# Kernel tuning notes

Hardware: AMD Instinct MI355X
Metric: run time of the kernel (lower is better)

The kernel has to match this reference:

```python
import jax, jax.numpy as jnp
import numpy as np

NEG_BIG = -(2.0 ** 32) + 1.0  # padding value used in Normal_attention


def setup_inputs() -> dict:
    key = jax.random.key(0)
    ks = jax.random.split(key, 9)
    U, V, kIL, kUI, B, L = 100000, 100001, 64, 64, 16384, 50
    IL = jax.random.normal(ks[0], (4, V, kIL), jnp.float32) * 0.01
    IL = IL.at[:, -1, :].set(0.0)  # padding_idx=-1 row zeroed
    LI = jax.random.normal(ks[1], (4, V, kIL), jnp.float32)
    LI = LI.at[:, -1, :].set(0.0)
    UI = jax.random.normal(ks[2], (4, U, kUI), jnp.float32)
    IU = jax.random.normal(ks[3], (V, kUI), jnp.float32) * 0.01
    IU = IU.at[-1, :].set(0.0)
    alpha = jnp.full((4,), 0.5, jnp.float32)
    uid = jax.random.randint(ks[4], (B,), 0, U)
    baskets = jax.random.randint(ks[5], (4, B, L), 0, V - 1)
    iid = jax.random.randint(ks[6], (4, B), 0, V - 1)
    neg_iid = jax.random.randint(ks[7], (4, B), 0, V - 1)
    return dict(IL=IL, LI=LI, UI=UI, IU=IU, alpha=alpha,
                uid=uid, baskets=baskets, iid=iid, neg_iid=neg_iid)


def _attend_score(x, tgt):
    # x: [B,4,k] aggregated period sequence; tgt: [P,B,k] target item embeddings
    k = x.shape[-1]
    w = jnp.einsum('bsk,pbk->pbs', x, tgt) / jnp.sqrt(jnp.asarray(k, x.dtype))
    w = jnp.where(w == 0.0, jnp.asarray(NEG_BIG, x.dtype), w)  # mask exact zeros (padding)
    w = jax.nn.softmax(w, axis=-1)                              # softmax over seq dim (4)
    # multiply input by attention weight, then bmm with target and sum over seq
    return jnp.einsum('bsk,pbs,pbk->pb', x, w, tgt)


def reference(IL, LI, UI, IU, alpha, uid, baskets, iid, neg_iid):
    n_items = LI.shape[1] - 1
    # aggregate: mean-pool each period's basket embedding -> [B,4,k]
    emb = jax.vmap(lambda W, idx: W[idx])(LI, baskets)          # [4,B,L,k]
    pad_mask = (baskets != n_items)[..., None].astype(emb.dtype)
    x = jnp.transpose(jnp.mean(emb * pad_mask, axis=2), (1, 0, 2))  # [B,4,k]

    tgt_pos = jax.vmap(lambda W, idx: W[idx])(IL, iid)          # [4,B,k]
    tgt_neg = jax.vmap(lambda W, idx: W[idx])(IL, neg_iid)      # [4,B,k]
    attn_pos = _attend_score(x, tgt_pos)                        # [4,B]
    attn_neg = _attend_score(x, tgt_neg)

    u = jax.vmap(lambda W: W[uid])(UI)                          # [4,B,kUI]
    mf_pos = jnp.sum(u * IU[iid], axis=-1)                      # [4,B]
    mf_neg = jnp.sum(u * IU[neg_iid], axis=-1)

    s = jax.nn.sigmoid(alpha)[:, None]                          # [4,1]
    pos = s * attn_pos + (1.0 - s) * mf_pos
    neg = s * attn_neg + (1.0 - s) * mf_neg
    return (pos[0], neg[0], pos[1], neg[1], pos[2], neg[2], pos[3], neg[3])
```

## Files before the change

### kernel.cpp

```cpp
#include <hip/hip_runtime.h>
#include <hip/hip_bf16.h>
#include <math.h>


#define NEG_BIG_F (-4294967295.0f)

typedef float v2f __attribute__((ext_vector_type(2)));

template<int CTRL, int RM>
__device__ __forceinline__ float dpp_add(float v) {
    int moved = __builtin_amdgcn_update_dpp(0, __float_as_int(v), CTRL, RM, 0xf, false);
    return v + __int_as_float(moved);
}

__device__ __forceinline__ float rsum64(float v) {
    v = dpp_add<0x121, 0xf>(v);
    v = dpp_add<0x122, 0xf>(v);
    v = dpp_add<0x124, 0xf>(v);
    v = dpp_add<0x128, 0xf>(v);
    v = dpp_add<0x142, 0xa>(v);
    v = dpp_add<0x143, 0xc>(v);
    return __int_as_float(__builtin_amdgcn_readlane(__float_as_int(v), 63));
}

__device__ __forceinline__ float plswap_add32(float a, float b) {
    auto r = __builtin_amdgcn_permlane32_swap(__float_as_uint(a), __float_as_uint(b),
                                              false, false);
    return __uint_as_float(r[0]) + __uint_as_float(r[1]);
}
__device__ __forceinline__ float plswap_add16(float a, float b) {
    auto r = __builtin_amdgcn_permlane16_swap(__float_as_uint(a), __float_as_uint(b),
                                              false, false);
    return __uint_as_float(r[0]) + __uint_as_float(r[1]);
}

__global__ __launch_bounds__(256) void convert_li_fp8(
    const float* __restrict__ src, unsigned int* __restrict__ dst, long n8)
{
    long i = (long)blockIdx.x * blockDim.x + threadIdx.x;
    const long stride = (long)gridDim.x * blockDim.x;
    for (; i < n8; i += stride) {
        float4 a = ((const float4*)src)[2 * i];
        float4 b = ((const float4*)src)[2 * i + 1];
        int w0 = __builtin_amdgcn_cvt_pk_fp8_f32(a.x, a.y, 0, false);
        w0     = __builtin_amdgcn_cvt_pk_fp8_f32(a.z, a.w, w0, true);
        int w1 = __builtin_amdgcn_cvt_pk_fp8_f32(b.x, b.y, 0, false);
        w1     = __builtin_amdgcn_cvt_pk_fp8_f32(b.z, b.w, w1, true);
        int2 o; o.x = w0; o.y = w1;
        ((int2*)dst)[i] = o;
    }
}

template<bool USE_FP8>
__global__ __launch_bounds__(256) void neuraltmt_kernel(
    const float* __restrict__ IL, const float* __restrict__ LI,
    const float* __restrict__ UI, const float* __restrict__ IU,
    const float* __restrict__ alpha,
    const int* __restrict__ uid, const int* __restrict__ baskets,
    const int* __restrict__ iid, const int* __restrict__ neg_iid,
    const unsigned char* __restrict__ T,
    float* __restrict__ out,
    int Bn, int V, int Ln, int U)
{
    const int b    = blockIdx.x;
    const int lane = threadIdx.x & 63;
    const int w    = threadIdx.x >> 6;
    const int n_items = V - 1;

    __shared__ float xs[4][64];

    const int* bk = baskets + ((size_t)w * Bn + b) * (size_t)Ln;

    if (USE_FP8 && Ln <= 64) {
        const unsigned char* Ts = T + (size_t)w * V * 64;
        int my_idx = (lane < Ln) ? bk[lane] : n_items;
        const int rs = lane >> 3;
        const int kq = lane & 7;

        int2 q[8];
        #pragma unroll
        for (int j = 0; j < 8; ++j) {
            if (8 * j < Ln) {
                int idx = __shfl(my_idx, 8 * j + rs, 64);
                q[j] = *(const int2*)(Ts + (((size_t)(unsigned)idx) << 6) + (kq << 3));
            }
        }
        float acc[8] = {0.f,0.f,0.f,0.f,0.f,0.f,0.f,0.f};
        #pragma unroll
        for (int j = 0; j < 8; ++j) {
            if (8 * j < Ln) {
                v2f d0 = __builtin_amdgcn_cvt_pk_f32_fp8(q[j].x, false);
                v2f d1 = __builtin_amdgcn_cvt_pk_f32_fp8(q[j].x, true);
                v2f d2 = __builtin_amdgcn_cvt_pk_f32_fp8(q[j].y, false);
                v2f d3 = __builtin_amdgcn_cvt_pk_f32_fp8(q[j].y, true);
                acc[0] += d0.x; acc[1] += d0.y; acc[2] += d1.x; acc[3] += d1.y;
                acc[4] += d2.x; acc[5] += d2.y; acc[6] += d3.x; acc[7] += d3.y;
            }
        }
        float s0 = plswap_add32(acc[0], acc[1]);
        float s1 = plswap_add32(acc[2], acc[3]);
        float s2 = plswap_add32(acc[4], acc[5]);
        float s3 = plswap_add32(acc[6], acc[7]);
        float t0 = plswap_add16(s0, s1);
        float t1 = plswap_add16(s2, s3);
        t0 = dpp_add<0x128, 0xf>(t0);
        t1 = dpp_add<0x128, 0xf>(t1);
        if (((lane >> 3) & 1) == 0) {
            const float invL = 1.0f / (float)Ln;
            const int g  = (lane >> 4) & 3;
            const int Ag = ((g & 1) << 1) | (g >> 1);
            const int kb = ((lane & 7) << 3) + Ag;
            xs[w][kb]     = t0 * invL;
            xs[w][kb + 4] = t1 * invL;
        }
    } else {
        const float* LIs = LI + (size_t)w * V * 64;
        const int rq = lane >> 4, kq = lane & 15;
        int my_idx = (lane < Ln && lane < 64) ? bk[lane] : n_items;
        float4 acc = make_float4(0.f, 0.f, 0.f, 0.f);
        const int lcap    = (Ln < 64) ? Ln : 64;
        const int ngroups = (lcap + 3) >> 2;
        int g = 0;
        for (; g + 4 <= ngroups; g += 4) {
            float4 v[4];
            #pragma unroll
            for (int j = 0; j < 4; ++j) {
                int idx = __shfl(my_idx, 4 * (g + j) + rq, 64);
                v[j] = *(const float4*)(LIs + (((size_t)(unsigned)idx) << 6) + (kq << 2));
            }
            #pragma unroll
            for (int j = 0; j < 4; ++j) {
                acc.x += v[j].x; acc.y += v[j].y; acc.z += v[j].z; acc.w += v[j].w;
            }
        }
        for (; g < ngroups; ++g) {
            int idx = __shfl(my_idx, 4 * g + rq, 64);
            float4 vv = *(const float4*)(LIs + (((size_t)(unsigned)idx) << 6) + (kq << 2));
            acc.x += vv.x; acc.y += vv.y; acc.z += vv.z; acc.w += vv.w;
        }
        for (int l = 64; l < Ln; ++l) {
            int idx = bk[l];
            float4 vv = *(const float4*)(LIs + (((size_t)(unsigned)idx) << 6) + (kq << 2));
            float m = (rq == 0) ? 1.0f : 0.0f;
            acc.x += m * vv.x; acc.y += m * vv.y; acc.z += m * vv.z; acc.w += m * vv.w;
        }
        #pragma unroll
        for (int off = 16; off <= 32; off <<= 1) {
            acc.x += __shfl_xor(acc.x, off, 64);
            acc.y += __shfl_xor(acc.y, off, 64);
            acc.z += __shfl_xor(acc.z, off, 64);
            acc.w += __shfl_xor(acc.w, off, 64);
        }
        if (lane < 16) {
            const float invL = 1.0f / (float)Ln;
            float4 xv = make_float4(acc.x * invL, acc.y * invL, acc.z * invL, acc.w * invL);
            *(float4*)&xs[w][lane << 2] = xv;
        }
    }
    __syncthreads();

    const int p = w;
    const float a  = alpha[p];
    const float sg = 1.0f / (1.0f + expf(-a));

    const int ip  = iid[(size_t)p * Bn + b];
    const int in_ = neg_iid[(size_t)p * Bn + b];
    const int u   = uid[b];

    const float* ILp = IL + (size_t)p * V * 64;
    const float tpos = ILp[(size_t)ip  * 64 + lane];
    const float tneg = ILp[(size_t)in_ * 64 + lane];
    const float uv   = UI[((size_t)p * U + u) * 64 + lane];
    const float iup  = IU[(size_t)ip  * 64 + lane];
    const float iun  = IU[(size_t)in_ * 64 + lane];

    float dpos[4], dneg[4];
    #pragma unroll
    for (int s = 0; s < 4; ++s) {
        float xv = xs[s][lane];
        dpos[s] = rsum64(xv * tpos);
        dneg[s] = rsum64(xv * tneg);
    }

    auto attend = [&](const float d[4]) -> float {
        float wv[4], m = -INFINITY;
        #pragma unroll
        for (int s = 0; s < 4; ++s) {
            wv[s] = (d[s] == 0.0f) ? NEG_BIG_F : d[s] * 0.125f;
            m = fmaxf(m, wv[s]);
        }
        float den = 0.0f, num = 0.0f;
        #pragma unroll
        for (int s = 0; s < 4; ++s) {
            float e = expf(wv[s] - m);
            den += e;
            num += e * d[s];
        }
        return num / den;
    };
    const float attn_pos = attend(dpos);
    const float attn_neg = attend(dneg);

    float mp = rsum64(uv * iup);
    float mn = rsum64(uv * iun);

    if (lane == 0) {
        float pos = sg * attn_pos + (1.0f - sg) * mp;
        float neg = sg * attn_neg + (1.0f - sg) * mn;
        out[(size_t)(2 * p)     * Bn + b] = pos;
        out[(size_t)(2 * p + 1) * Bn + b] = neg;
    }
}

extern "C" void kernel_launch(void* const* d_in, const int* in_sizes, int n_in,
                              void* d_out, int out_size, void* d_ws, size_t ws_size,
                              hipStream_t stream) {
    const float* IL      = (const float*)d_in[0];
    const float* LI      = (const float*)d_in[1];
    const float* UI      = (const float*)d_in[2];
    const float* IU      = (const float*)d_in[3];
    const float* alpha   = (const float*)d_in[4];
    const int*   uid     = (const int*)d_in[5];
    const int*   baskets = (const int*)d_in[6];
    const int*   iid     = (const int*)d_in[7];
    const int*   neg_iid = (const int*)d_in[8];

    const int Bn = in_sizes[5];
    const int V  = in_sizes[3] / 64;
    const int U  = in_sizes[2] / (4 * 64);
    const int Ln = in_sizes[6] / (4 * Bn);

    float* out = (float*)d_out;

    const long  nLI  = (long)4 * V * 64;
    const size_t need = (size_t)nLI;
    const bool use_fp8 = (d_ws != nullptr) && (ws_size >= need);

    if (use_fp8) {
        unsigned char* T = (unsigned char*)d_ws;
        convert_li_fp8<<<4096, 256, 0, stream>>>(LI, (unsigned int*)T, nLI / 8);
        neuraltmt_kernel<true><<<Bn, 256, 0, stream>>>(
            IL, LI, UI, IU, alpha, uid, baskets, iid, neg_iid, T, out, Bn, V, Ln, U);
    } else {
        neuraltmt_kernel<false><<<Bn, 256, 0, stream>>>(
            IL, LI, UI, IU, alpha, uid, baskets, iid, neg_iid, nullptr, out, Bn, V, Ln, U);
    }
}
```

Before: 330.0 us.

## Hoist target loads before basket gather and batch wave reductions with permlane swaps

Moves the index and target/user embedding loads ahead of the basket aggregation so their latency overlaps the gather instead of sitting after the barrier. Replaces the ten separate full-wave DPP reductions with combined permlane32/16 swap reductions that pack several dot products into one wave and read them out by lane. Switches the FP8 accumulation to packed two-wide vector adds. This cuts reduction instruction count and exposed load latency, at the cost of more live registers across the aggregation phase.

```diff
diff --git a/kernel.cpp b/kernel.cpp
--- a/kernel.cpp
+++ b/kernel.cpp
@@ -13,16 +13,6 @@
     return v + __int_as_float(moved);
 }
 
-__device__ __forceinline__ float rsum64(float v) {
-    v = dpp_add<0x121, 0xf>(v);
-    v = dpp_add<0x122, 0xf>(v);
-    v = dpp_add<0x124, 0xf>(v);
-    v = dpp_add<0x128, 0xf>(v);
-    v = dpp_add<0x142, 0xa>(v);
-    v = dpp_add<0x143, 0xc>(v);
-    return __int_as_float(__builtin_amdgcn_readlane(__float_as_int(v), 63));
-}
-
 __device__ __forceinline__ float plswap_add32(float a, float b) {
     auto r = __builtin_amdgcn_permlane32_swap(__float_as_uint(a), __float_as_uint(b),
                                               false, false);
@@ -32,6 +22,10 @@
     auto r = __builtin_amdgcn_permlane16_swap(__float_as_uint(a), __float_as_uint(b),
                                               false, false);
     return __uint_as_float(r[0]) + __uint_as_float(r[1]);
+}
+
+__device__ __forceinline__ float rl(float v, int lane) {
+    return __int_as_float(__builtin_amdgcn_readlane(__float_as_int(v), lane));
 }
 
 __global__ __launch_bounds__(256) void convert_li_fp8(
@@ -70,10 +64,22 @@
     __shared__ float xs[4][64];
 
     const int* bk = baskets + ((size_t)w * Bn + b) * (size_t)Ln;
+    int my_idx = (lane < Ln) ? bk[lane] : n_items;
+
+    const int p   = w;
+    const int ip  = iid[(size_t)p * Bn + b];
+    const int in_ = neg_iid[(size_t)p * Bn + b];
+    const int u   = uid[b];
+
+    const float* ILp = IL + (size_t)p * V * 64;
+    const float tpos = ILp[(size_t)ip  * 64 + lane];
+    const float tneg = ILp[(size_t)in_ * 64 + lane];
+    const float uv   = UI[((size_t)p * U + u) * 64 + lane];
+    const float iup  = IU[(size_t)ip  * 64 + lane];
+    const float iun  = IU[(size_t)in_ * 64 + lane];
 
     if (USE_FP8 && Ln <= 64) {
         const unsigned char* Ts = T + (size_t)w * V * 64;
-        int my_idx = (lane < Ln) ? bk[lane] : n_items;
         const int rs = lane >> 3;
         const int kq = lane & 7;
 
@@ -85,22 +91,20 @@
                 q[j] = *(const int2*)(Ts + (((size_t)(unsigned)idx) << 6) + (kq << 3));
             }
         }
-        float acc[8] = {0.f,0.f,0.f,0.f,0.f,0.f,0.f,0.f};
+        v2f a01 = {0.f, 0.f}, a23 = {0.f, 0.f}, a45 = {0.f, 0.f}, a67 = {0.f, 0.f};
         #pragma unroll
         for (int j = 0; j < 8; ++j) {
             if (8 * j < Ln) {
-                v2f d0 = __builtin_amdgcn_cvt_pk_f32_fp8(q[j].x, false);
-                v2f d1 = __builtin_amdgcn_cvt_pk_f32_fp8(q[j].x, true);
-                v2f d2 = __builtin_amdgcn_cvt_pk_f32_fp8(q[j].y, false);
-                v2f d3 = __builtin_amdgcn_cvt_pk_f32_fp8(q[j].y, true);
-                acc[0] += d0.x; acc[1] += d0.y; acc[2] += d1.x; acc[3] += d1.y;
-                acc[4] += d2.x; acc[5] += d2.y; acc[6] += d3.x; acc[7] += d3.y;
-            }
-        }
-        float s0 = plswap_add32(acc[0], acc[1]);
-        float s1 = plswap_add32(acc[2], acc[3]);
-        float s2 = plswap_add32(acc[4], acc[5]);
-        float s3 = plswap_add32(acc[6], acc[7]);
+                a01 += __builtin_amdgcn_cvt_pk_f32_fp8(q[j].x, false);
+                a23 += __builtin_amdgcn_cvt_pk_f32_fp8(q[j].x, true);
+                a45 += __builtin_amdgcn_cvt_pk_f32_fp8(q[j].y, false);
+                a67 += __builtin_amdgcn_cvt_pk_f32_fp8(q[j].y, true);
+            }
+        }
+        float s0 = plswap_add32(a01.x, a01.y);
+        float s1 = plswap_add32(a23.x, a23.y);
+        float s2 = plswap_add32(a45.x, a45.y);
+        float s3 = plswap_add32(a67.x, a67.y);
         float t0 = plswap_add16(s0, s1);
         float t1 = plswap_add16(s2, s3);
         t0 = dpp_add<0x128, 0xf>(t0);
@@ -116,7 +120,6 @@
     } else {
         const float* LIs = LI + (size_t)w * V * 64;
         const int rq = lane >> 4, kq = lane & 15;
-        int my_idx = (lane < Ln && lane < 64) ? bk[lane] : n_items;
         float4 acc = make_float4(0.f, 0.f, 0.f, 0.f);
         const int lcap    = (Ln < 64) ? Ln : 64;
         const int ngroups = (lcap + 3) >> 2;
@@ -159,28 +162,37 @@
     }
     __syncthreads();
 
-    const int p = w;
     const float a  = alpha[p];
     const float sg = 1.0f / (1.0f + expf(-a));
 
-    const int ip  = iid[(size_t)p * Bn + b];
-    const int in_ = neg_iid[(size_t)p * Bn + b];
-    const int u   = uid[b];
-
-    const float* ILp = IL + (size_t)p * V * 64;
-    const float tpos = ILp[(size_t)ip  * 64 + lane];
-    const float tneg = ILp[(size_t)in_ * 64 + lane];
-    const float uv   = UI[((size_t)p * U + u) * 64 + lane];
-    const float iup  = IU[(size_t)ip  * 64 + lane];
-    const float iun  = IU[(size_t)in_ * 64 + lane];
-
-    float dpos[4], dneg[4];
+    float xp[4], xn[4];
     #pragma unroll
     for (int s = 0; s < 4; ++s) {
         float xv = xs[s][lane];
-        dpos[s] = rsum64(xv * tpos);
-        dneg[s] = rsum64(xv * tneg);
-    }
+        xp[s] = xv * tpos;
+        xn[s] = xv * tneg;
+    }
+    float A  = plswap_add32(xp[0], xp[1]);
+    float Bv = plswap_add32(xp[2], xp[3]);
+    float C  = plswap_add32(xn[0], xn[1]);
+    float D  = plswap_add32(xn[2], xn[3]);
+    float E  = plswap_add16(A, Bv);
+    float F  = plswap_add16(C, D);
+    E = dpp_add<0x121, 0xf>(E); E = dpp_add<0x122, 0xf>(E);
+    E = dpp_add<0x124, 0xf>(E); E = dpp_add<0x128, 0xf>(E);
+    F = dpp_add<0x121, 0xf>(F); F = dpp_add<0x122, 0xf>(F);
+    F = dpp_add<0x124, 0xf>(F); F = dpp_add<0x128, 0xf>(F);
+
+    float dpos[4], dneg[4];
+    dpos[0] = rl(E, 0); dpos[2] = rl(E, 16); dpos[1] = rl(E, 32); dpos[3] = rl(E, 48);
+    dneg[0] = rl(F, 0); dneg[2] = rl(F, 16); dneg[1] = rl(F, 32); dneg[3] = rl(F, 48);
+
+    float M = plswap_add32(uv * iup, uv * iun);
+    M = dpp_add<0x121, 0xf>(M); M = dpp_add<0x122, 0xf>(M);
+    M = dpp_add<0x124, 0xf>(M); M = dpp_add<0x128, 0xf>(M);
+    M = dpp_add<0x142, 0xa>(M);
+    float mp = rl(M, 31);
+    float mn = rl(M, 63);
 
     auto attend = [&](const float d[4]) -> float {
         float wv[4], m = -INFINITY;
@@ -200,9 +212,6 @@
     };
     const float attn_pos = attend(dpos);
     const float attn_neg = attend(dneg);
-
-    float mp = rsum64(uv * iup);
-    float mn = rsum64(uv * iun);
 
     if (lane == 0) {
         float pos = sg * attn_pos + (1.0f - sg) * mp;
```

Result: faster. 320.9 us (-2.7%).
